# Performance work log

Measured on AMD Instinct MI355X. Metric: run time of the kernel, lower is better.

## Reference

```python
import jax, jax.numpy as jnp
import numpy as np

N = 50000   # nodes per graph
E = 800000  # edges per graph
BN_EPS = 1e-5


def _bn_relu(h, g, b):
    # BatchNorm1d in training mode (biased variance over the node axis) + ReLU
    m = h.mean(0)
    v = ((h - m) ** 2).mean(0)
    return jax.nn.relu((h - m) * jax.lax.rsqrt(v + BN_EPS) * g + b)


def _gin(x, edge, W, b, g=None, beta=None):
    # PyG GINConv with eps=0: h = MLP((1+eps)*x + sum_{j->i} x_j)
    agg = jax.ops.segment_sum(x[edge[0]], edge[1], num_segments=x.shape[0])
    h = (x + agg) @ W.T + b
    if g is None:
        return jax.nn.relu(h)  # recon blocks: Linear + ReLU (dropout=0)
    return _bn_relu(h, g, beta)  # align/extractor blocks: Linear + BN + ReLU


def setup_inputs() -> dict:
    key = jax.random.key(0)
    ks = iter(jax.random.split(key, 16))

    def lin(k, out_d, in_d):
        s = 1.0 / np.sqrt(in_d)
        return jax.random.uniform(k, (out_d, in_d), jnp.float32, -s, s)

    inp = {}
    inp["ft0"] = jax.random.normal(next(ks), (N, 256), jnp.float32)
    inp["ft1"] = jax.random.normal(next(ks), (N, 128), jnp.float32)
    inp["fs"] = jax.random.normal(next(ks), (N, 256), jnp.float32)
    inp["et0"] = jax.random.randint(next(ks), (2, E), 0, N, jnp.int32)
    inp["et1"] = jax.random.randint(next(ks), (2, E), 0, N, jnp.int32)
    inp["es"] = jax.random.randint(next(ks), (2, E), 0, N, jnp.int32)
    # align_teachers[i]: Linear(ch_t, 128) + BN(128)
    inp["aT0_W"] = lin(next(ks), 128, 256)
    inp["aT0_b"] = jnp.zeros((128,), jnp.float32)
    inp["aT0_g"] = jnp.ones((128,), jnp.float32)
    inp["aT0_beta"] = jnp.zeros((128,), jnp.float32)
    inp["aT1_W"] = lin(next(ks), 128, 128)
    inp["aT1_b"] = jnp.zeros((128,), jnp.float32)
    inp["aT1_g"] = jnp.ones((128,), jnp.float32)
    inp["aT1_beta"] = jnp.zeros((128,), jnp.float32)
    # align_student: Linear(256, 128) + BN(128)
    inp["aS_W"] = lin(next(ks), 128, 256)
    inp["aS_b"] = jnp.zeros((128,), jnp.float32)
    inp["aS_g"] = jnp.ones((128,), jnp.float32)
    inp["aS_beta"] = jnp.zeros((128,), jnp.float32)
    # extractor: Linear(128, 64) + BN(64), shared across graphs
    inp["ext_W"] = lin(next(ks), 64, 128)
    inp["ext_b"] = jnp.zeros((64,), jnp.float32)
    inp["ext_g"] = jnp.ones((64,), jnp.float32)
    inp["ext_beta"] = jnp.zeros((64,), jnp.float32)
    # recon_teachers[i]: Linear(64, ch_t), no BN
    inp["rT0_W"] = lin(next(ks), 256, 64)
    inp["rT0_b"] = jnp.zeros((256,), jnp.float32)
    inp["rT1_W"] = lin(next(ks), 128, 64)
    inp["rT1_b"] = jnp.zeros((128,), jnp.float32)
    return inp


def reference(ft0, ft1, fs, et0, et1, es,
              aT0_W, aT0_b, aT0_g, aT0_beta,
              aT1_W, aT1_b, aT1_g, aT1_beta,
              aS_W, aS_b, aS_g, aS_beta,
              ext_W, ext_b, ext_g, ext_beta,
              rT0_W, rT0_b, rT1_W, rT1_b):
    a0 = _gin(ft0, et0, aT0_W, aT0_b, aT0_g, aT0_beta)   # [N, 128]
    a1 = _gin(ft1, et1, aT1_W, aT1_b, aT1_g, aT1_beta)   # [N, 128]
    a_s = _gin(fs, es, aS_W, aS_b, aS_g, aS_beta)        # [N, 128]
    h0 = _gin(a0, et0, ext_W, ext_b, ext_g, ext_beta)    # [N, 64]
    h1 = _gin(a1, et1, ext_W, ext_b, ext_g, ext_beta)    # [N, 64]
    hs = _gin(a_s, es, ext_W, ext_b, ext_g, ext_beta)    # [N, 64]
    f0 = _gin(h0, et0, rT0_W, rT0_b)                     # [N, 256]
    f1 = _gin(h1, et1, rT1_W, rT1_b)                     # [N, 128]
    ht = jnp.concatenate([h0, h1], axis=0)               # [2N, 64]
    return (hs, ht, f0, f1)
```

## Files before the change

### kernel.cpp

```cpp
#include <hip/hip_runtime.h>
#include <hip/hip_bf16.h>

#define CPE 8192

typedef short short8 __attribute__((ext_vector_type(8)));
typedef float f32x4 __attribute__((ext_vector_type(4)));
using u16 = unsigned short;

__device__ __forceinline__ float bf2f(u16 u) {
    return __uint_as_float(((unsigned)u) << 16);
}
__device__ __forceinline__ u16 f2bf(float f) {
    __hip_bfloat16 h = __float2bfloat16(f);
    return *reinterpret_cast<u16*>(&h);
}

__global__ void k_wcvt6(const float* w0, const float* w1, const float* w2,
                        const float* w3, const float* w4, const float* w5,
                        u16* __restrict__ out,
                        int s0, int s1, int s2, int s3, int s4, int s5) {
    int i = blockIdx.x * blockDim.x + threadIdx.x;
    int b0 = s0, b1 = b0 + s1, b2 = b1 + s2, b3 = b2 + s3, b4 = b3 + s4, b5 = b4 + s5;
    if (i >= b5) return;
    const float* w;
    int o;
    if (i < b0) { w = w0; o = i; }
    else if (i < b1) { w = w1; o = i - b0; }
    else if (i < b2) { w = w2; o = i - b1; }
    else if (i < b3) { w = w3; o = i - b2; }
    else if (i < b4) { w = w4; o = i - b3; }
    else { w = w5; o = i - b4; }
    out[i] = f2bf(w[o]);
}


__global__ void k_p1(const int* __restrict__ e0, const int* __restrict__ e1,
                     const int* __restrict__ e2, int* __restrict__ cnt,
                     int E, int nC, int NB) {
    __shared__ int h[256];
    int g = blockIdx.x / nC, c = blockIdx.x - g * nC;
    const int* dst = (g == 0 ? e0 : g == 1 ? e1 : e2) + E;
    for (int b = threadIdx.x; b < NB; b += 256) h[b] = 0;
    __syncthreads();
    int lo = c * CPE, hi = min(E, lo + CPE);
    for (int e = lo + threadIdx.x; e < hi; e += 256)
        atomicAdd(&h[dst[e] >> 8], 1);
    __syncthreads();
    for (int b = threadIdx.x; b < NB; b += 256)
        cnt[((long)g * NB + b) * nC + c] = h[b];
}

__global__ void k_p2a(const int* __restrict__ cnt, int* __restrict__ tot, int nC) {
    __shared__ int s[256];
    long gb = blockIdx.x;
    const int* row = cnt + gb * nC;
    int v = 0;
    for (int c = threadIdx.x; c < nC; c += 256) v += row[c];
    s[threadIdx.x] = v;
    __syncthreads();
    for (int o = 128; o > 0; o >>= 1) {
        if (threadIdx.x < o) s[threadIdx.x] += s[threadIdx.x + o];
        __syncthreads();
    }
    if (threadIdx.x == 0) tot[gb] = s[0];
}

__global__ void k_p2b(const int* __restrict__ tot, int* __restrict__ baseE,
                      int* __restrict__ rowptr, int E, int N, int NB) {
    __shared__ int s[256];
    int g = blockIdx.x, t = threadIdx.x;
    int v = (t < NB) ? tot[g * NB + t] : 0;
    s[t] = v;
    __syncthreads();
    for (int o = 1; o < 256; o <<= 1) {
        int a = (t >= o) ? s[t - o] : 0;
        __syncthreads();
        s[t] += a;
        __syncthreads();
    }
    if (t < NB) baseE[g * (NB + 1) + t] = s[t] - v;
    if (t == 0) {
        baseE[g * (NB + 1) + NB] = E;
        rowptr[(long)g * (N + 1) + N] = E;
    }
}

__global__ void k_p2c(const int* __restrict__ cnt, const int* __restrict__ baseE,
                      int* __restrict__ ofs, int nC, int NB) {
    __shared__ int s[256];
    long gb = blockIdx.x;
    int g = (int)(gb / NB), b = (int)(gb - (long)g * NB);
    int t = threadIdx.x;
    int v = (t < nC) ? cnt[gb * nC + t] : 0;
    s[t] = v;
    __syncthreads();
    for (int o = 1; o < 256; o <<= 1) {
        int a = (t >= o) ? s[t - o] : 0;
        __syncthreads();
        s[t] += a;
        __syncthreads();
    }
    if (t < nC) ofs[gb * nC + t] = baseE[g * (NB + 1) + b] + s[t] - v;
}

__global__ void k_p3(const int* __restrict__ e0, const int* __restrict__ e1,
                     const int* __restrict__ e2, const int* __restrict__ ofs,
                     unsigned* __restrict__ part, int E, int nC, int NB) {
    __shared__ int lbase[256];
    __shared__ int lcur[256];
    int g = blockIdx.x / nC, c = blockIdx.x - g * nC;
    const int* eg = (g == 0 ? e0 : g == 1 ? e1 : e2);
    const int* src = eg;
    const int* dst = eg + E;
    for (int b = threadIdx.x; b < NB; b += 256) {
        lbase[b] = ofs[((long)g * NB + b) * nC + c];
        lcur[b] = 0;
    }
    __syncthreads();
    int lo = c * CPE, hi = min(E, lo + CPE);
    unsigned* pg = part + (long)g * E;
    for (int e = lo + threadIdx.x; e < hi; e += 256) {
        int d = dst[e];
        int b = d >> 8;
        int pos = lbase[b] + atomicAdd(&lcur[b], 1);
        pg[pos] = ((unsigned)(d & 255) << 16) | (unsigned)src[e];
    }
}

__global__ void k_p4(const unsigned* __restrict__ part, const int* __restrict__ baseE,
                     int* __restrict__ rowptr, int* __restrict__ srcs,
                     int E, int N, int NB) {
    __shared__ int h[256];
    __shared__ int s[256];
    __shared__ int cur[256];
    int g = blockIdx.x / NB, b = blockIdx.x - g * NB;
    int n0 = b << 8;
    int nn = min(256, N - n0);
    int lo = baseE[g * (NB + 1) + b], hi = baseE[g * (NB + 1) + b + 1];
    int t = threadIdx.x;
    h[t] = 0;
    __syncthreads();
    const unsigned* pg = part + (long)g * E;
    for (int i = lo + t; i < hi; i += 256)
        atomicAdd(&h[pg[i] >> 16], 1);
    __syncthreads();
    int v = h[t];
    s[t] = v;
    __syncthreads();
    for (int o = 1; o < 256; o <<= 1) {
        int a = (t >= o) ? s[t - o] : 0;
        __syncthreads();
        s[t] += a;
        __syncthreads();
    }
    int excl = lo + s[t] - v;
    if (t < nn) rowptr[(long)g * (N + 1) + n0 + t] = excl;
    cur[t] = excl;
    __syncthreads();
    int* sg = srcs + (long)g * E;
    for (int i = lo + t; i < hi; i += 256) {
        unsigned r = pg[i];
        int pos = atomicAdd(&cur[r >> 16], 1);
        sg[pos] = (int)(r & 0xFFFFu);
    }
}

template <bool ABF, bool BN_IN, bool RELU_OUT, bool BF16_OUT>
__device__ __forceinline__ void gemm_body(const void* X, const float* stats,
                                          const u16* __restrict__ Wb,
                                          const float* __restrict__ bias,
                                          void* Yv, int MT, int Cin, int SH,
                                          int wl, int l) {
    int mt = wl >> SH;
    if (mt >= MT) return;
    int CG = 1 << SH;
    int COUT = CG * 64;
    int cg = wl & (CG - 1);
    int lm = l & 15, lh = l >> 4;
    int kb = lh * 8;

    const float* xrf = nullptr;
    const u16* xrb = nullptr;
    if (ABF) xrb = (const u16*)X + (long)(mt * 16 + lm) * Cin + kb;
    else     xrf = (const float*)X + (long)(mt * 16 + lm) * Cin + kb;
    const u16* wp[4];
#pragma unroll
    for (int t = 0; t < 4; ++t)
        wp[t] = Wb + (long)(cg * 64 + t * 16 + lm) * Cin + kb;
    const float* scp = nullptr;
    const float* shp = nullptr;
    if (BN_IN) {
        scp = stats + 2 * Cin + kb;
        shp = stats + 3 * Cin + kb;
    }

    f32x4 acc[4];
#pragma unroll
    for (int t = 0; t < 4; ++t) acc[t] = (f32x4){0.f, 0.f, 0.f, 0.f};

    for (int k0 = 0; k0 < Cin; k0 += 32) {
        short8 a;
        if (ABF) {
            short8 raw = *reinterpret_cast<const short8*>(xrb);
            if (BN_IN) {
#pragma unroll
                for (int j = 0; j < 8; ++j) {
                    float x = bf2f((u16)raw[j]);
                    x = fmaxf(fmaf(x, scp[j], shp[j]), 0.f);
                    a[j] = (short)f2bf(x);
                }
                scp += 32; shp += 32;
            } else {
                a = raw;
            }
            xrb += 32;
        } else {
            float4 x0 = *reinterpret_cast<const float4*>(xrf);
            float4 x1 = *reinterpret_cast<const float4*>(xrf + 4);
            a[0] = (short)f2bf(x0.x); a[1] = (short)f2bf(x0.y);
            a[2] = (short)f2bf(x0.z); a[3] = (short)f2bf(x0.w);
            a[4] = (short)f2bf(x1.x); a[5] = (short)f2bf(x1.y);
            a[6] = (short)f2bf(x1.z); a[7] = (short)f2bf(x1.w);
            xrf += 32;
        }
#pragma unroll
        for (int t = 0; t < 4; ++t) {
            short8 b = *reinterpret_cast<const short8*>(wp[t]);
            acc[t] = __builtin_amdgcn_mfma_f32_16x16x32_bf16(a, b, acc[t], 0, 0, 0);
            wp[t] += 32;
        }
    }

    int nb = mt * 16 + lh * 4;
#pragma unroll
    for (int t = 0; t < 4; ++t) {
        int col = cg * 64 + t * 16 + lm;
        float bi = bias[col];
#pragma unroll
        for (int r = 0; r < 4; ++r) {
            float v = acc[t][r] + bi;
            if (RELU_OUT) v = fmaxf(v, 0.f);
            if (BF16_OUT)
                ((u16*)Yv)[(long)(nb + r) * COUT + col] = f2bf(v);
            else
                ((float*)Yv)[(long)(nb + r) * COUT + col] = v;
        }
    }
}

template <int CIN>
__device__ __forceinline__ void gemmL1T_body(const float* __restrict__ X,
                                             const u16* __restrict__ Wb,
                                             const float* __restrict__ bias,
                                             u16* __restrict__ Yb,
                                             int N, int row0, int tid, u16* As) {
    constexpr int LGC = (CIN == 256) ? 8 : 7;
    constexpr int ITERS = (64 * CIN) / (256 * 4);
#pragma unroll
    for (int i = 0; i < ITERS; ++i) {
        int f = i * 1024 + tid * 4;
        int row = f >> LGC;
        int col = f & (CIN - 1);
        int grow = row0 + row;
        float4 x = make_float4(0.f, 0.f, 0.f, 0.f);
        if (grow < N) x = *reinterpret_cast<const float4*>(X + (long)grow * CIN + col);
        ushort4 b = make_ushort4(f2bf(x.x), f2bf(x.y), f2bf(x.z), f2bf(x.w));
        int byte = (row << (LGC + 1)) + col * 2;
        byte ^= ((row & 7) << 4);
        *reinterpret_cast<ushort4*>(reinterpret_cast<char*>(As) + byte) = b;
    }
    __syncthreads();

    int w = tid >> 6, l = tid & 63;
    int lm = l & 15, lh = l >> 4;
    int lr = w * 16 + lm;
    int kb = lh * 8;
    const u16* wb = Wb + (long)lm * CIN + kb;

    f32x4 acc[8];
#pragma unroll
    for (int t = 0; t < 8; ++t) acc[t] = (f32x4){0.f, 0.f, 0.f, 0.f};

#pragma unroll
    for (int k0 = 0; k0 < CIN; k0 += 32) {
        int byte = (lr << (LGC + 1)) + (k0 + kb) * 2;
        byte ^= ((lr & 7) << 4);
        short8 a = *reinterpret_cast<const short8*>(reinterpret_cast<char*>(As) + byte);
#pragma unroll
        for (int t = 0; t < 8; ++t) {
            short8 b = *reinterpret_cast<const short8*>(wb + (long)t * 16 * CIN + k0);
            acc[t] = __builtin_amdgcn_mfma_f32_16x16x32_bf16(a, b, acc[t], 0, 0, 0);
        }
    }

    int nb = row0 + w * 16 + lh * 4;
#pragma unroll
    for (int t = 0; t < 8; ++t) {
        int col = t * 16 + lm;
        float bi = bias[col];
#pragma unroll
        for (int r = 0; r < 4; ++r) {
            if (nb + r < N)
                Yb[(long)(nb + r) * 128 + col] = f2bf(acc[t][r] + bi);
        }
    }
}

__global__ __launch_bounds__(256) void k_gemmL1(
        const float* x0, const float* x1, const float* x2,
        const u16* w0, const u16* w1, const u16* w2,
        const float* b0, const float* b1, const float* b2,
        u16* Yb, int N, int B1) {
    __shared__ u16 As[64 * 256];
    int g = blockIdx.x / B1;
    int row0 = (blockIdx.x - g * B1) * 64;
    int tid = threadIdx.x;
    if (g == 0)
        gemmL1T_body<256>(x0, w0, b0, Yb, N, row0, tid, As);
    else if (g == 1)
        gemmL1T_body<128>(x1, w1, b1, Yb + (long)N * 128, N, row0, tid, As);
    else
        gemmL1T_body<256>(x2, w2, b2, Yb + (long)N * 256, N, row0, tid, As);
}

__global__ __launch_bounds__(256) void k_gemmL2(
        const u16* Hb, const float* ST, const u16* wext, const float* bext,
        u16* Yb, int MT, int N, int B2) {
    int g = blockIdx.x / B2;
    int wl = (blockIdx.x - g * B2) * 4 + (threadIdx.x >> 6);
    gemm_body<true, true, false, true>(Hb + (long)g * N * 128, ST + g * 512, wext,
                                       bext, Yb + (long)g * N * 64, MT, 128, 0,
                                       wl, threadIdx.x & 63);
}

__global__ __launch_bounds__(256) void k_gemmL3(
        const u16* h3, const u16* wr0, const u16* wr1,
        const float* br0, const float* br1,
        float* f0, float* f1, int MT, int N, int B0) {
    int b = blockIdx.x;
    int g = (b < B0) ? 0 : 1;
    int wl = (g == 0 ? b : b - B0) * 4 + (threadIdx.x >> 6);
    if (g == 0)
        gemm_body<true, false, true, false>(h3, nullptr, wr0, br0, f0, MT, 64, 2,
                                            wl, threadIdx.x & 63);
    else
        gemm_body<true, false, true, false>(h3 + (long)N * 64, nullptr, wr1, br1,
                                            f1, MT, 64, 1, wl, threadIdx.x & 63);
}

template <int CH>
__global__ void k_aggb3(const u16* __restrict__ in, const int* __restrict__ rp,
                        const int* __restrict__ sr, u16* __restrict__ outb,
                        int N, int E, int BPG) {
    int g = blockIdx.x / BPG;
    int bb = blockIdx.x - g * BPG;
    int l = threadIdx.x & 63;
    int ll = l & 31;
    int n = (bb << 3) + ((threadIdx.x >> 6) << 1) + (l >> 5);
    if (n >= N) return;
    const int* rowptr = rp + (long)g * (N + 1);
    const int* srcs = sr + (long)g * E;
    int p = rowptr[n], p1 = rowptr[n + 1];
    if constexpr (CH == 128) {
        const ushort4* Yp = reinterpret_cast<const ushort4*>(in + (long)g * N * 128) + ll;
        ushort4 a = Yp[(long)n << 5];
        float s0 = bf2f(a.x), s1 = bf2f(a.y), s2 = bf2f(a.z), s3 = bf2f(a.w);
        while (p + 8 <= p1) {
            ushort4 r[8];
#pragma unroll
            for (int j = 0; j < 8; ++j) r[j] = Yp[(long)srcs[p + j] << 5];
#pragma unroll
            for (int j = 0; j < 8; ++j) {
                s0 += bf2f(r[j].x); s1 += bf2f(r[j].y);
                s2 += bf2f(r[j].z); s3 += bf2f(r[j].w);
            }
            p += 8;
        }
        while (p < p1) {
            ushort4 r = Yp[(long)srcs[p] << 5];
            s0 += bf2f(r.x); s1 += bf2f(r.y); s2 += bf2f(r.z); s3 += bf2f(r.w);
            ++p;
        }
        ushort4 o = make_ushort4(f2bf(s0), f2bf(s1), f2bf(s2), f2bf(s3));
        (reinterpret_cast<ushort4*>(outb + (long)g * N * 128) + ll)[(long)n << 5] = o;
    } else {
        const unsigned* Yp = reinterpret_cast<const unsigned*>(in + (long)g * N * 64) + ll;
        unsigned a = Yp[(long)n << 5];
        float s0 = bf2f((u16)a), s1 = bf2f((u16)(a >> 16));
        while (p + 8 <= p1) {
            unsigned r[8];
#pragma unroll
            for (int j = 0; j < 8; ++j) r[j] = Yp[(long)srcs[p + j] << 5];
#pragma unroll
            for (int j = 0; j < 8; ++j) {
                s0 += bf2f((u16)r[j]);
                s1 += bf2f((u16)(r[j] >> 16));
            }
            p += 8;
        }
        while (p < p1) {
            unsigned r = Yp[(long)srcs[p] << 5];
            s0 += bf2f((u16)r);
            s1 += bf2f((u16)(r >> 16));
            ++p;
        }
        unsigned o = (unsigned)f2bf(s0) | ((unsigned)f2bf(s1) << 16);
        (reinterpret_cast<unsigned*>(outb + (long)g * N * 64) + ll)[(long)n << 5] = o;
    }
}

template <int C>
__global__ void k_bnstats1(const u16* __restrict__ h, float* __restrict__ parts,
                           int N, int PSTRIDE) {
    constexpr int RPB = 256 / C;
    constexpr int LGC = (C == 128) ? 7 : 6;
    __shared__ float ts[256], ts2[256];
    int g = blockIdx.x >> 8;
    int blk = blockIdx.x & 255;
    const u16* hg = h + (long)g * N * C;
    float* pg = parts + (long)g * PSTRIDE;
    int tid = threadIdx.x;
    int c = tid & (C - 1);
    float s = 0.f, s2 = 0.f;
    for (int n = blk * RPB + (tid >> LGC); n < N; n += 256 * RPB) {
        float v = bf2f(hg[((long)n << LGC) + c]);
        s += v;
        s2 = fmaf(v, v, s2);
    }
    ts[tid] = s;
    ts2[tid] = s2;
    __syncthreads();
    if (tid < C) {
#pragma unroll
        for (int i = 1; i < RPB; ++i) {
            s += ts[tid + i * C];
            s2 += ts2[tid + i * C];
        }
        pg[blk * 2 * C + tid] = s;
        pg[blk * 2 * C + C + tid] = s2;
    }
}

template <int C>
__global__ void k_bnstats2(const float* __restrict__ parts,
                           const float* g0, const float* g1, const float* g2,
                           const float* b0, const float* b1, const float* b2,
                           float* __restrict__ ST, float invN, int PSTRIDE) {
    int g = blockIdx.x;
    const float* gam = g == 0 ? g0 : (g == 1 ? g1 : g2);
    const float* bet = g == 0 ? b0 : (g == 1 ? b1 : b2);
    const float* pg = parts + (long)g * PSTRIDE;
    float* st = ST + g * 4 * C;
    int c = threadIdx.x;
    float s = 0.f, s2 = 0.f;
    for (int b = 0; b < 256; ++b) {
        s += pg[b * 2 * C + c];
        s2 += pg[b * 2 * C + C + c];
    }
    float m = s * invN;
    float v = s2 * invN - m * m;
    float sc = gam[c] * rsqrtf(v + 1e-5f);
    st[2 * C + c] = sc;
    st[3 * C + c] = bet[c] - m * sc;
}

__global__ void k_bnapply3(const u16* __restrict__ h2b, const float* __restrict__ ST2,
                           float* __restrict__ out, u16* __restrict__ obb,
                           int N, int BPG) {
    int g = blockIdx.x / BPG;
    int idx = (blockIdx.x - g * BPG) * 256 + threadIdx.x;
    if (idx >= N * 16) return;
    int n = idx >> 4;
    int c4 = (idx & 15) << 2;
    const u16* hg = h2b + (long)g * N * 64;
    const float* st = ST2 + g * 256;
    ushort4 hv = *reinterpret_cast<const ushort4*>(hg + ((long)n << 6) + c4);
    const float4 sc = *reinterpret_cast<const float4*>(st + 128 + c4);
    const float4 sh = *reinterpret_cast<const float4*>(st + 192 + c4);
    float4 o;
    o.x = fmaxf(fmaf(bf2f(hv.x), sc.x, sh.x), 0.f);
    o.y = fmaxf(fmaf(bf2f(hv.y), sc.y, sh.y), 0.f);
    o.z = fmaxf(fmaf(bf2f(hv.z), sc.z, sh.z), 0.f);
    o.w = fmaxf(fmaf(bf2f(hv.w), sc.w, sh.w), 0.f);
    float* yb = (g == 0) ? out + (long)N * 64 : (g == 1) ? out + (long)N * 128 : out;
    *reinterpret_cast<float4*>(yb + ((long)n << 6) + c4) = o;
    if (g < 2) {
        ushort4 ob = make_ushort4(f2bf(o.x), f2bf(o.y), f2bf(o.z), f2bf(o.w));
        *reinterpret_cast<ushort4*>(obb + (long)g * N * 64 + ((long)n << 6) + c4) = ob;
    }
}

static inline int cdiv(long a, int b) { return (int)((a + b - 1) / b); }

extern "C" void kernel_launch(void* const* d_in, const int* in_sizes, int n_in,
                              void* d_out, int out_size, void* d_ws, size_t ws_size,
                              hipStream_t stream) {
    const float* ft0 = (const float*)d_in[0];
    const float* ft1 = (const float*)d_in[1];
    const float* fs  = (const float*)d_in[2];
    const int* et0 = (const int*)d_in[3];
    const int* et1 = (const int*)d_in[4];
    const int* es  = (const int*)d_in[5];
    const float* aT0_W = (const float*)d_in[6];
    const float* aT0_b = (const float*)d_in[7];
    const float* aT0_g = (const float*)d_in[8];
    const float* aT0_be = (const float*)d_in[9];
    const float* aT1_W = (const float*)d_in[10];
    const float* aT1_b = (const float*)d_in[11];
    const float* aT1_g = (const float*)d_in[12];
    const float* aT1_be = (const float*)d_in[13];
    const float* aS_W = (const float*)d_in[14];
    const float* aS_b = (const float*)d_in[15];
    const float* aS_g = (const float*)d_in[16];
    const float* aS_be = (const float*)d_in[17];
    const float* ext_W = (const float*)d_in[18];
    const float* ext_b = (const float*)d_in[19];
    const float* ext_g = (const float*)d_in[20];
    const float* ext_be = (const float*)d_in[21];
    const float* rT0_W = (const float*)d_in[22];
    const float* rT0_b = (const float*)d_in[23];
    const float* rT1_W = (const float*)d_in[24];
    const float* rT1_b = (const float*)d_in[25];

    const int N = in_sizes[0] / 256;
    const int E = in_sizes[3] / 2;
    const int NB = cdiv(N, 256);
    const int nC = cdiv(E, CPE);
    const int MT = N / 16;

    float* out = (float*)d_out;
    float* o_f0 = out + (long)N * 192;
    float* o_f1 = out + (long)N * 448;

    char* p = (char*)d_ws;
    u16* Yb  = (u16*)p;        p += (size_t)3 * N * 128 * 2;
    u16* Hb  = (u16*)p;        p += (size_t)3 * N * 128 * 2;
    u16* h2b = (u16*)p;        p += (size_t)3 * N * 64 * 2;
    u16* obb = (u16*)p;        p += (size_t)2 * N * 64 * 2;
    int* rp   = (int*)p;       p += (size_t)3 * (N + 1) * 4;
    int* sr   = (int*)p;       p += (size_t)3 * E * 4;
    unsigned* part = (unsigned*)p; p += (size_t)3 * E * 4;
    int* cnt  = (int*)p;       p += (size_t)3 * NB * nC * 4;
    int* ofs  = (int*)p;       p += (size_t)3 * NB * nC * 4;
    int* tot  = (int*)p;       p += (size_t)3 * NB * 4;
    int* baseE = (int*)p;      p += (size_t)3 * (NB + 1) * 4;
    u16* WBF = (u16*)p;        p += (size_t)(256*128 + 128*128 + 256*128 + 128*64 + 64*256 + 64*128) * 2;
    float* ST1 = (float*)p;    p += (size_t)3 * 512 * 4;
    float* ST2 = (float*)p;    p += (size_t)3 * 256 * 4;
    float* PARTS = (float*)p;  p += (size_t)3 * 256 * 256 * 4;

    u16* aT0b = WBF;
    u16* aT1b = aT0b + 256 * 128;
    u16* aSb  = aT1b + 128 * 128;
    u16* extb = aSb + 256 * 128;
    u16* rT0b = extb + 128 * 64;
    u16* rT1b = rT0b + 64 * 256;

    k_p1<<<3 * nC, 256, 0, stream>>>(et0, et1, es, cnt, E, nC, NB);
    k_p2a<<<3 * NB, 256, 0, stream>>>(cnt, tot, nC);
    k_p2b<<<3, 256, 0, stream>>>(tot, baseE, rp, E, N, NB);
    k_p2c<<<3 * NB, 256, 0, stream>>>(cnt, baseE, ofs, nC, NB);
    k_p3<<<3 * nC, 256, 0, stream>>>(et0, et1, es, ofs, part, E, nC, NB);
    k_p4<<<3 * NB, 256, 0, stream>>>(part, baseE, rp, sr, E, N, NB);

    {
        int tot_w = 256*128 + 128*128 + 256*128 + 128*64 + 64*256 + 64*128;
        k_wcvt6<<<cdiv(tot_w, 256), 256, 0, stream>>>(
            aT0_W, aT1_W, aS_W, ext_W, rT0_W, rT1_W, WBF,
            256*128, 128*128, 256*128, 128*64, 64*256, 64*128);
    }

    const int B1 = cdiv(N, 64);
    const int B2 = cdiv(MT, 4);
    const int BPG = N / 8;
    const int BPA = cdiv((long)N * 16, 256);

    k_gemmL1<<<3 * B1, 256, 0, stream>>>(ft0, ft1, fs, aT0b, aT1b, aSb,
                                         aT0_b, aT1_b, aS_b, Yb, N, B1);
    k_aggb3<128><<<3 * BPG, 256, 0, stream>>>(Yb, rp, sr, Hb, N, E, BPG);
    k_bnstats1<128><<<3 * 256, 256, 0, stream>>>(Hb, PARTS, N, 256 * 256);
    k_bnstats2<128><<<3, 128, 0, stream>>>(PARTS, aT0_g, aT1_g, aS_g,
                                           aT0_be, aT1_be, aS_be, ST1, 1.0f / N, 256 * 256);

    k_gemmL2<<<3 * B2, 256, 0, stream>>>(Hb, ST1, extb, ext_b, Yb, MT, N, B2);
    k_aggb3<64><<<3 * BPG, 256, 0, stream>>>(Yb, rp, sr, h2b, N, E, BPG);
    k_bnstats1<64><<<3 * 256, 256, 0, stream>>>(h2b, PARTS, N, 256 * 128);
    k_bnstats2<64><<<3, 64, 0, stream>>>(PARTS, ext_g, ext_g, ext_g,
                                         ext_be, ext_be, ext_be, ST2, 1.0f / N, 256 * 128);
    k_bnapply3<<<3 * BPA, 256, 0, stream>>>(h2b, ST2, out, obb, N, BPA);

    k_aggb3<64><<<2 * BPG, 256, 0, stream>>>(obb, rp, sr, h2b, N, E, BPG);
    k_gemmL3<<<MT + cdiv((long)MT * 2, 4), 256, 0, stream>>>(
        h2b, rT0b, rT1b, rT0_b, rT1_b, o_f0, o_f1, MT, N, MT);
}
```

Measured before the change: 517.9 us.

## Stage L1 weights in LDS and double-buffer four row tiles per block

The first-layer GEMM now copies the bf16 weight matrix into swizzled LDS once per block, and each block processes 256 rows as four 64-row tiles instead of one. The next tile's fp32 rows are loaded into registers while MFMAs run on the current tile, then converted and written to the other LDS buffer. This removes repeated global/L2 weight reads and overlaps activation loads with compute. In exchange each block uses about 128 KB of LDS, which lowers occupancy, and the grid is four times smaller. Workspace pointers are also aligned to 16 bytes so the vector weight loads are safe.

```diff
diff --git a/kernel.cpp b/kernel.cpp
--- a/kernel.cpp
+++ b/kernel.cpp
@@ -249,60 +249,102 @@
 }
 
 template <int CIN>
-__device__ __forceinline__ void gemmL1T_body(const float* __restrict__ X,
-                                             const u16* __restrict__ Wb,
-                                             const float* __restrict__ bias,
-                                             u16* __restrict__ Yb,
-                                             int N, int row0, int tid, u16* As) {
+__device__ __forceinline__ void gemmL1v4(const float* __restrict__ X,
+                                         const u16* __restrict__ Wb,
+                                         const float* __restrict__ bias,
+                                         u16* __restrict__ Yb,
+                                         int N, int m0, int tid, u16* S) {
     constexpr int LGC = (CIN == 256) ? 8 : 7;
-    constexpr int ITERS = (64 * CIN) / (256 * 4);
-#pragma unroll
-    for (int i = 0; i < ITERS; ++i) {
+    constexpr int ABUF = 64 * CIN;
+    constexpr int WITER = (128 * CIN) / (256 * 8);
+    constexpr int AITER = (64 * CIN) / (256 * 4);
+    u16* Ws = S;
+    u16* As = S + 128 * CIN;
+
+#pragma unroll
+    for (int i = 0; i < WITER; ++i) {
+        int e = (i * 256 + tid) * 8;
+        int wr = e >> LGC;
+        int wc = e & (CIN - 1);
+        short8 v = *reinterpret_cast<const short8*>(Wb + e);
+        int byte = (((wr << LGC) + wc) * 2) ^ ((wr & 7) << 4);
+        *reinterpret_cast<short8*>(reinterpret_cast<char*>(Ws) + byte) = v;
+    }
+
+    float4 r[AITER];
+#pragma unroll
+    for (int i = 0; i < AITER; ++i) {
         int f = i * 1024 + tid * 4;
-        int row = f >> LGC;
-        int col = f & (CIN - 1);
-        int grow = row0 + row;
-        float4 x = make_float4(0.f, 0.f, 0.f, 0.f);
-        if (grow < N) x = *reinterpret_cast<const float4*>(X + (long)grow * CIN + col);
-        ushort4 b = make_ushort4(f2bf(x.x), f2bf(x.y), f2bf(x.z), f2bf(x.w));
-        int byte = (row << (LGC + 1)) + col * 2;
-        byte ^= ((row & 7) << 4);
+        int row = f >> LGC, col = f & (CIN - 1);
+        int gr = m0 + row;
+        r[i] = (gr < N) ? *reinterpret_cast<const float4*>(X + (long)gr * CIN + col)
+                        : make_float4(0.f, 0.f, 0.f, 0.f);
+    }
+#pragma unroll
+    for (int i = 0; i < AITER; ++i) {
+        int f = i * 1024 + tid * 4;
+        int row = f >> LGC, col = f & (CIN - 1);
+        int byte = (((row << LGC) + col) * 2) ^ ((row & 7) << 4);
+        ushort4 b = make_ushort4(f2bf(r[i].x), f2bf(r[i].y), f2bf(r[i].z), f2bf(r[i].w));
         *reinterpret_cast<ushort4*>(reinterpret_cast<char*>(As) + byte) = b;
     }
     __syncthreads();
 
     int w = tid >> 6, l = tid & 63;
     int lm = l & 15, lh = l >> 4;
-    int lr = w * 16 + lm;
     int kb = lh * 8;
-    const u16* wb = Wb + (long)lm * CIN + kb;
-
-    f32x4 acc[8];
-#pragma unroll
-    for (int t = 0; t < 8; ++t) acc[t] = (f32x4){0.f, 0.f, 0.f, 0.f};
-
-#pragma unroll
-    for (int k0 = 0; k0 < CIN; k0 += 32) {
-        int byte = (lr << (LGC + 1)) + (k0 + kb) * 2;
-        byte ^= ((lr & 7) << 4);
-        short8 a = *reinterpret_cast<const short8*>(reinterpret_cast<char*>(As) + byte);
+    int lr = (w << 4) + lm;
+
+#pragma unroll
+    for (int s = 0; s < 4; ++s) {
+        u16* buf = As + (s & 1) * ABUF;
+        if (s < 3) {
+#pragma unroll
+            for (int i = 0; i < AITER; ++i) {
+                int f = i * 1024 + tid * 4;
+                int row = f >> LGC, col = f & (CIN - 1);
+                int gr = m0 + (s + 1) * 64 + row;
+                r[i] = (gr < N) ? *reinterpret_cast<const float4*>(X + (long)gr * CIN + col)
+                                : make_float4(0.f, 0.f, 0.f, 0.f);
+            }
+        }
+        f32x4 acc[8];
+#pragma unroll
+        for (int t = 0; t < 8; ++t) acc[t] = (f32x4){0.f, 0.f, 0.f, 0.f};
+#pragma unroll
+        for (int k0 = 0; k0 < CIN; k0 += 32) {
+            int abyte = (((lr << LGC) + k0 + kb) * 2) ^ ((lr & 7) << 4);
+            short8 a = *reinterpret_cast<const short8*>(reinterpret_cast<char*>(buf) + abyte);
+#pragma unroll
+            for (int t = 0; t < 8; ++t) {
+                int wr = (t << 4) + lm;
+                int bbyte = (((wr << LGC) + k0 + kb) * 2) ^ ((wr & 7) << 4);
+                short8 b = *reinterpret_cast<const short8*>(reinterpret_cast<char*>(Ws) + bbyte);
+                acc[t] = __builtin_amdgcn_mfma_f32_16x16x32_bf16(a, b, acc[t], 0, 0, 0);
+            }
+        }
+        int nb = m0 + s * 64 + (w << 4) + lh * 4;
 #pragma unroll
         for (int t = 0; t < 8; ++t) {
-            short8 b = *reinterpret_cast<const short8*>(wb + (long)t * 16 * CIN + k0);
-            acc[t] = __builtin_amdgcn_mfma_f32_16x16x32_bf16(a, b, acc[t], 0, 0, 0);
-        }
-    }
-
-    int nb = row0 + w * 16 + lh * 4;
-#pragma unroll
-    for (int t = 0; t < 8; ++t) {
-        int col = t * 16 + lm;
-        float bi = bias[col];
-#pragma unroll
-        for (int r = 0; r < 4; ++r) {
-            if (nb + r < N)
-                Yb[(long)(nb + r) * 128 + col] = f2bf(acc[t][r] + bi);
-        }
+            int col = (t << 4) + lm;
+            float bi = bias[col];
+#pragma unroll
+            for (int rr = 0; rr < 4; ++rr)
+                if (nb + rr < N)
+                    Yb[(long)(nb + rr) * 128 + col] = f2bf(acc[t][rr] + bi);
+        }
+        if (s < 3) {
+            u16* nbuf = As + ((s + 1) & 1) * ABUF;
+#pragma unroll
+            for (int i = 0; i < AITER; ++i) {
+                int f = i * 1024 + tid * 4;
+                int row = f >> LGC, col = f & (CIN - 1);
+                int byte = (((row << LGC) + col) * 2) ^ ((row & 7) << 4);
+                ushort4 b = make_ushort4(f2bf(r[i].x), f2bf(r[i].y), f2bf(r[i].z), f2bf(r[i].w));
+                *reinterpret_cast<ushort4*>(reinterpret_cast<char*>(nbuf) + byte) = b;
+            }
+        }
+        __syncthreads();
     }
 }
 
@@ -311,16 +353,16 @@
         const u16* w0, const u16* w1, const u16* w2,
         const float* b0, const float* b1, const float* b2,
         u16* Yb, int N, int B1) {
-    __shared__ u16 As[64 * 256];
+    __shared__ __align__(16) u16 S[128 * 256 + 2 * 64 * 256];
     int g = blockIdx.x / B1;
-    int row0 = (blockIdx.x - g * B1) * 64;
+    int m0 = (blockIdx.x - g * B1) * 256;
     int tid = threadIdx.x;
     if (g == 0)
-        gemmL1T_body<256>(x0, w0, b0, Yb, N, row0, tid, As);
+        gemmL1v4<256>(x0, w0, b0, Yb, N, m0, tid, S);
     else if (g == 1)
-        gemmL1T_body<128>(x1, w1, b1, Yb + (long)N * 128, N, row0, tid, As);
+        gemmL1v4<128>(x1, w1, b1, Yb + (long)N * 128, N, m0, tid, S);
     else
-        gemmL1T_body<256>(x2, w2, b2, Yb + (long)N * 256, N, row0, tid, As);
+        gemmL1v4<256>(x2, w2, b2, Yb + (long)N * 256, N, m0, tid, S);
 }
 
 __global__ __launch_bounds__(256) void k_gemmL2(
@@ -533,6 +575,7 @@
     float* o_f1 = out + (long)N * 448;
 
     char* p = (char*)d_ws;
+    auto align16 = [&]() { p = (char*)(((uintptr_t)p + 15) & ~(uintptr_t)15); };
     u16* Yb  = (u16*)p;        p += (size_t)3 * N * 128 * 2;
     u16* Hb  = (u16*)p;        p += (size_t)3 * N * 128 * 2;
     u16* h2b = (u16*)p;        p += (size_t)3 * N * 64 * 2;
@@ -544,7 +587,9 @@
     int* ofs  = (int*)p;       p += (size_t)3 * NB * nC * 4;
     int* tot  = (int*)p;       p += (size_t)3 * NB * 4;
     int* baseE = (int*)p;      p += (size_t)3 * (NB + 1) * 4;
+    align16();
     u16* WBF = (u16*)p;        p += (size_t)(256*128 + 128*128 + 256*128 + 128*64 + 64*256 + 64*128) * 2;
+    align16();
     float* ST1 = (float*)p;    p += (size_t)3 * 512 * 4;
     float* ST2 = (float*)p;    p += (size_t)3 * 256 * 4;
     float* PARTS = (float*)p;  p += (size_t)3 * 256 * 256 * 4;
@@ -570,7 +615,7 @@
             256*128, 128*128, 256*128, 128*64, 64*256, 64*128);
     }
 
-    const int B1 = cdiv(N, 64);
+    const int B1 = cdiv(N, 256);
     const int B2 = cdiv(MT, 4);
     const int BPG = N / 8;
     const int BPA = cdiv((long)N * 16, 256);
```

Result: slower. 557.9 us (+7.7%).

## Stage layer-1 GEMM weights in LDS and process 256 rows per block

Applied to the files above, without the earlier changes.

The first-layer GIN GEMM now copies 128-column slices of the bf16 weight matrix into swizzled shared memory and reads B fragments from LDS instead of global memory. Each block covers four 64-row subtiles (256 rows), so there are a quarter as many blocks. The intent is to cut repeated global/L2 weight reads. The cost is that the weight slice is reloaded for every subtile, there are extra barriers, and fewer blocks are available for load balancing. Workspace pointers are also 16-byte aligned so the vector loads of the weights are safe.

```diff
diff --git a/kernel.cpp b/kernel.cpp
--- a/kernel.cpp
+++ b/kernel.cpp
@@ -249,59 +249,70 @@
 }
 
 template <int CIN>
-__device__ __forceinline__ void gemmL1T_body(const float* __restrict__ X,
-                                             const u16* __restrict__ Wb,
-                                             const float* __restrict__ bias,
-                                             u16* __restrict__ Yb,
-                                             int N, int row0, int tid, u16* As) {
-    constexpr int LGC = (CIN == 256) ? 8 : 7;
-    constexpr int ITERS = (64 * CIN) / (256 * 4);
-#pragma unroll
-    for (int i = 0; i < ITERS; ++i) {
-        int f = i * 1024 + tid * 4;
-        int row = f >> LGC;
-        int col = f & (CIN - 1);
-        int grow = row0 + row;
-        float4 x = make_float4(0.f, 0.f, 0.f, 0.f);
-        if (grow < N) x = *reinterpret_cast<const float4*>(X + (long)grow * CIN + col);
-        ushort4 b = make_ushort4(f2bf(x.x), f2bf(x.y), f2bf(x.z), f2bf(x.w));
-        int byte = (row << (LGC + 1)) + col * 2;
-        byte ^= ((row & 7) << 4);
-        *reinterpret_cast<ushort4*>(reinterpret_cast<char*>(As) + byte) = b;
-    }
-    __syncthreads();
-
+__device__ __forceinline__ void gemmL1v5(const float* __restrict__ X,
+                                         const u16* __restrict__ Wb,
+                                         const float* __restrict__ bias,
+                                         u16* __restrict__ Yb,
+                                         int N, int m0, int tid, u16* S) {
+    constexpr int KH = CIN / 128;
+    u16* Ws = S;
+    u16* As = S + 128 * 128;
     int w = tid >> 6, l = tid & 63;
     int lm = l & 15, lh = l >> 4;
-    int lr = w * 16 + lm;
     int kb = lh * 8;
-    const u16* wb = Wb + (long)lm * CIN + kb;
-
-    f32x4 acc[8];
-#pragma unroll
-    for (int t = 0; t < 8; ++t) acc[t] = (f32x4){0.f, 0.f, 0.f, 0.f};
-
-#pragma unroll
-    for (int k0 = 0; k0 < CIN; k0 += 32) {
-        int byte = (lr << (LGC + 1)) + (k0 + kb) * 2;
-        byte ^= ((lr & 7) << 4);
-        short8 a = *reinterpret_cast<const short8*>(reinterpret_cast<char*>(As) + byte);
+    int lr = (w << 4) + lm;
+
+#pragma unroll
+    for (int s = 0; s < 4; ++s) {
+        f32x4 acc[8];
+#pragma unroll
+        for (int t = 0; t < 8; ++t) acc[t] = (f32x4){0.f, 0.f, 0.f, 0.f};
+
+#pragma unroll
+        for (int kh = 0; kh < KH; ++kh) {
+#pragma unroll
+            for (int i = 0; i < 8; ++i) {
+                int e = (i * 256 + tid) * 8;
+                int wr = e >> 7, wc = e & 127;
+                short8 v = *reinterpret_cast<const short8*>(Wb + (long)wr * CIN + kh * 128 + wc);
+                int byte = (((wr << 7) + wc) * 2) ^ ((wr & 7) << 4);
+                *reinterpret_cast<short8*>(reinterpret_cast<char*>(Ws) + byte) = v;
+            }
+#pragma unroll
+            for (int i = 0; i < 8; ++i) {
+                int f = i * 1024 + tid * 4;
+                int row = f >> 7, col = f & 127;
+                int gr = m0 + s * 64 + row;
+                float4 x = make_float4(0.f, 0.f, 0.f, 0.f);
+                if (gr < N) x = *reinterpret_cast<const float4*>(X + (long)gr * CIN + kh * 128 + col);
+                ushort4 b = make_ushort4(f2bf(x.x), f2bf(x.y), f2bf(x.z), f2bf(x.w));
+                int byte = (((row << 7) + col) * 2) ^ ((row & 7) << 4);
+                *reinterpret_cast<ushort4*>(reinterpret_cast<char*>(As) + byte) = b;
+            }
+            __syncthreads();
+#pragma unroll
+            for (int k0 = 0; k0 < 128; k0 += 32) {
+                int abyte = (((lr << 7) + k0 + kb) * 2) ^ ((lr & 7) << 4);
+                short8 a = *reinterpret_cast<const short8*>(reinterpret_cast<char*>(As) + abyte);
+#pragma unroll
+                for (int t = 0; t < 8; ++t) {
+                    int wr2 = (t << 4) + lm;
+                    int bbyte = (((wr2 << 7) + k0 + kb) * 2) ^ ((wr2 & 7) << 4);
+                    short8 b = *reinterpret_cast<const short8*>(reinterpret_cast<char*>(Ws) + bbyte);
+                    acc[t] = __builtin_amdgcn_mfma_f32_16x16x32_bf16(a, b, acc[t], 0, 0, 0);
+                }
+            }
+            __syncthreads();
+        }
+        int nb = m0 + s * 64 + (w << 4) + lh * 4;
 #pragma unroll
         for (int t = 0; t < 8; ++t) {
-            short8 b = *reinterpret_cast<const short8*>(wb + (long)t * 16 * CIN + k0);
-            acc[t] = __builtin_amdgcn_mfma_f32_16x16x32_bf16(a, b, acc[t], 0, 0, 0);
-        }
-    }
-
-    int nb = row0 + w * 16 + lh * 4;
-#pragma unroll
-    for (int t = 0; t < 8; ++t) {
-        int col = t * 16 + lm;
-        float bi = bias[col];
-#pragma unroll
-        for (int r = 0; r < 4; ++r) {
-            if (nb + r < N)
-                Yb[(long)(nb + r) * 128 + col] = f2bf(acc[t][r] + bi);
+            int col = (t << 4) + lm;
+            float bi = bias[col];
+#pragma unroll
+            for (int rr = 0; rr < 4; ++rr)
+                if (nb + rr < N)
+                    Yb[(long)(nb + rr) * 128 + col] = f2bf(acc[t][rr] + bi);
         }
     }
 }
@@ -311,16 +322,16 @@
         const u16* w0, const u16* w1, const u16* w2,
         const float* b0, const float* b1, const float* b2,
         u16* Yb, int N, int B1) {
-    __shared__ u16 As[64 * 256];
+    __shared__ __align__(16) u16 S[128 * 128 + 64 * 128];
     int g = blockIdx.x / B1;
-    int row0 = (blockIdx.x - g * B1) * 64;
+    int m0 = (blockIdx.x - g * B1) * 256;
     int tid = threadIdx.x;
     if (g == 0)
-        gemmL1T_body<256>(x0, w0, b0, Yb, N, row0, tid, As);
+        gemmL1v5<256>(x0, w0, b0, Yb, N, m0, tid, S);
     else if (g == 1)
-        gemmL1T_body<128>(x1, w1, b1, Yb + (long)N * 128, N, row0, tid, As);
+        gemmL1v5<128>(x1, w1, b1, Yb + (long)N * 128, N, m0, tid, S);
     else
-        gemmL1T_body<256>(x2, w2, b2, Yb + (long)N * 256, N, row0, tid, As);
+        gemmL1v5<256>(x2, w2, b2, Yb + (long)N * 256, N, m0, tid, S);
 }
 
 __global__ __launch_bounds__(256) void k_gemmL2(
@@ -533,6 +544,7 @@
     float* o_f1 = out + (long)N * 448;
 
     char* p = (char*)d_ws;
+    auto align16 = [&]() { p = (char*)(((uintptr_t)p + 15) & ~(uintptr_t)15); };
     u16* Yb  = (u16*)p;        p += (size_t)3 * N * 128 * 2;
     u16* Hb  = (u16*)p;        p += (size_t)3 * N * 128 * 2;
     u16* h2b = (u16*)p;        p += (size_t)3 * N * 64 * 2;
@@ -544,7 +556,9 @@
     int* ofs  = (int*)p;       p += (size_t)3 * NB * nC * 4;
     int* tot  = (int*)p;       p += (size_t)3 * NB * 4;
     int* baseE = (int*)p;      p += (size_t)3 * (NB + 1) * 4;
+    align16();
     u16* WBF = (u16*)p;        p += (size_t)(256*128 + 128*128 + 256*128 + 128*64 + 64*256 + 64*128) * 2;
+    align16();
     float* ST1 = (float*)p;    p += (size_t)3 * 512 * 4;
     float* ST2 = (float*)p;    p += (size_t)3 * 256 * 4;
     float* PARTS = (float*)p;  p += (size_t)3 * 256 * 256 * 4;
@@ -570,7 +584,7 @@
             256*128, 128*128, 256*128, 128*64, 64*256, 64*128);
     }
 
-    const int B1 = cdiv(N, 64);
+    const int B1 = cdiv(N, 256);
     const int B2 = cdiv(MT, 4);
     const int BPG = N / 8;
     const int BPA = cdiv((long)N * 16, 256);
```

Result: slower. 532.6 us (+2.9%).
